# Kernel optimization log

Hardware: AMD Instinct MI355X
Metric: run time of the kernel (lower is better)

Reference implementation:

```python
import jax, jax.numpy as jnp
import numpy as np

N = 100_000
E = 1_600_000
D_IN, D_HID, D_OUT = 512, 256, 256


def setup_inputs() -> dict:
    key = jax.random.key(0)
    ks = jax.random.split(key, 10)
    x = jax.random.normal(ks[0], (N, D_IN), dtype=jnp.float32)
    edge_index = jax.random.randint(ks[1], (2, E), 0, N, dtype=jnp.int64)
    edge_weight = jax.random.uniform(ks[2], (E,), dtype=jnp.float32)
    # Glorot-ish init for the per-layer linear weights (PyG GCNConv: Linear w/o bias, bias added after aggregation)
    W1 = jax.random.normal(ks[3], (D_IN, D_HID), dtype=jnp.float32) * (1.0 / np.sqrt(D_IN))
    b1 = jnp.zeros((D_HID,), dtype=jnp.float32)
    W2 = jax.random.normal(ks[4], (D_HID, D_HID), dtype=jnp.float32) * (1.0 / np.sqrt(D_HID))
    b2 = jnp.zeros((D_HID,), dtype=jnp.float32)
    W3 = jax.random.normal(ks[5], (D_HID, D_OUT), dtype=jnp.float32) * (1.0 / np.sqrt(D_HID))
    b3 = jnp.zeros((D_OUT,), dtype=jnp.float32)
    return {"x": x, "edge_index": edge_index, "edge_weight": edge_weight,
            "W1": W1, "b1": b1, "W2": W2, "b2": b2, "W3": W3, "b3": b3}


def gcn_layer(h_in, W, b, row, col, ew, n):
    # PyG GCNConv with normalize=True, add_self_loops=True (fill value 1.0), aggr='add':
    # h = X W; deg[i] = sum of incoming edge weights (incl. self loop);
    # norm_e = deg^-1/2[row] * w_e * deg^-1/2[col]; out[col] += norm_e * h[row]; out += bias
    h = h_in @ W                                            # [n, d_out]
    deg = jnp.zeros((n,), h.dtype).at[col].add(ew) + 1.0    # +1 from self loop
    dinv = jnp.where(deg > 0, jax.lax.rsqrt(deg), 0.0)      # deg_inv_sqrt, inf -> 0
    norm = dinv[row] * ew * dinv[col]                       # [E]
    out = jnp.zeros_like(h).at[col].add(norm[:, None] * h[row])
    out = out + (dinv * dinv)[:, None] * h                  # self-loop contribution (norm_ii = dinv_i^2)
    return out + b


def reference(x, edge_index, edge_weight, W1, b1, W2, b2, W3, b3):
    row, col = edge_index[0], edge_index[1]
    n = x.shape[0]
    # dropout p=0.0 -> identity
    h = jax.nn.relu(gcn_layer(x, W1, b1, row, col, edge_weight, n))
    h = jax.nn.relu(gcn_layer(h, W2, b2, row, col, edge_weight, n))
    return gcn_layer(h, W3, b3, row, col, edge_weight, n)
```

## Files before the change

### kernel.cpp

```cpp
#include <hip/hip_runtime.h>
#include <hip/hip_bf16.h>


#define D 256
#define ELLW 48
#define BSH 7
#define CAP 2432

typedef unsigned short ushort_t;
typedef unsigned long long u64;
typedef float f32x4 __attribute__((ext_vector_type(4)));
typedef short bf16x8 __attribute__((ext_vector_type(8)));
typedef unsigned int u32x4 __attribute__((ext_vector_type(4)));
typedef int i32x4 __attribute__((ext_vector_type(4)));

__device__ __forceinline__ float blo(unsigned u) { return __uint_as_float(u << 16); }
__device__ __forceinline__ float bhi(unsigned u) { return __uint_as_float(u & 0xFFFF0000u); }
__device__ __forceinline__ ushort_t f2b(float f) {
    unsigned u = __float_as_uint(f);
    return (ushort_t)((u + 0x7FFFu + ((u >> 16) & 1u)) >> 16);
}
__device__ __forceinline__ void gload_lds16(const ushort_t* g, ushort_t* l) {
    __builtin_amdgcn_global_load_lds((const __attribute__((address_space(1))) unsigned int*)g,
                                     (__attribute__((address_space(3))) unsigned int*)l, 16, 0, 0);
}

__global__ __launch_bounds__(256) void bin_p1(const int* __restrict__ row,
                                              const int* __restrict__ col,
                                              const float* __restrict__ ew,
                                              int* __restrict__ bfill,
                                              i32x4* __restrict__ bins, int E) {
    int e = blockIdx.x * 256 + threadIdx.x;
    if (e < E) {
        int c = __builtin_nontemporal_load(&col[e]);
        int r = __builtin_nontemporal_load(&row[e]);
        float w = __builtin_nontemporal_load(&ew[e]);
        int b = c >> BSH;
        int pos = atomicAdd(&bfill[b * 16], 1);
        if (pos < CAP) {
            i32x4 rec = {r, __float_as_int(w), c, 0};
            __builtin_nontemporal_store(rec, &bins[(size_t)b * CAP + pos]);
        }
    }
}

__global__ __launch_bounds__(256) void bin_p2(const i32x4* __restrict__ bins,
                                              const int* __restrict__ bfill,
                                              int* __restrict__ cnt,
                                              float* __restrict__ dinv,
                                              u64* __restrict__ ell, int N) {
    __shared__ int scnt[1 << BSH];
    __shared__ float ssum[1 << BSH];
    const int b = blockIdx.x;
    const int base = b << BSH;
    const int t = threadIdx.x;
    if (t < (1 << BSH)) { scnt[t] = 0; ssum[t] = 0.f; }
    __syncthreads();
    int fill = bfill[b * 16];
    if (fill > CAP) fill = CAP;
    for (int i = t; i < fill; i += 256) {
        i32x4 rec = bins[(size_t)b * CAP + i];
        int li = rec.z - base;
        int pos = atomicAdd(&scnt[li], 1);
        if (pos < ELLW)
            ell[(size_t)rec.z * ELLW + pos] = ((u64)(unsigned)rec.y << 32) | (unsigned)rec.x;
        atomicAdd(&ssum[li], __int_as_float(rec.y));
    }
    __syncthreads();
    if (t < (1 << BSH)) {
        int node = base + t;
        if (node < N) {
            int m = scnt[t];
            cnt[node] = (m > ELLW) ? ELLW : m;
            dinv[node] = rsqrtf(ssum[t] + 1.0f);
        }
    }
}

__global__ __launch_bounds__(256) void cvtT_kernel(const float* __restrict__ W,
                                                   ushort_t* __restrict__ WT, int K, int C) {
    int i = blockIdx.x * 256 + threadIdx.x;
    if (i < K * C) {
        int c = i / K, k = i - c * K;
        WT[i] = f2b(W[(size_t)k * C + c]);
    }
}

template <int K, bool AF32>
__global__ __launch_bounds__(256) void gemm_mfma(const void* __restrict__ Ap,
                                                 const ushort_t* __restrict__ WT,
                                                 ushort_t* __restrict__ C, int nvalid) {
    __shared__ ushort_t As[128 * 64];
    __shared__ ushort_t Bs[256 * 64];
    const int tid = threadIdx.x;
    const int lane = tid & 63, wave = tid >> 6;
    const int wrow = wave >> 1, wcol = wave & 1;
    const int fr = lane & 15, fq = lane >> 4;
    const int r0 = blockIdx.x * 128;

    f32x4 acc[4][8] = {};

    for (int k0 = 0; k0 < K; k0 += 64) {
        if constexpr (AF32) {
            const float* Af = (const float*)Ap;
#pragma unroll
            for (int i = 0; i < 8; ++i) {
                int idx = i * 256 + tid;
                int rowt = idx >> 4;
                int c4 = idx & 15;
                int grow = r0 + rowt;
                if (grow >= nvalid) grow = nvalid - 1;
                f32x4 v = __builtin_nontemporal_load(
                    (const f32x4*)&Af[(size_t)grow * K + k0 + c4 * 4]);
                ushort4 h;
                h.x = f2b(v[0]); h.y = f2b(v[1]); h.z = f2b(v[2]); h.w = f2b(v[3]);
                int slot = c4 >> 1, half = c4 & 1;
                int off = rowt * 64 + ((slot ^ (rowt & 7)) << 3) + (half << 2);
                *(ushort4*)&As[off] = h;
            }
        } else {
            const ushort_t* Ab = (const ushort_t*)Ap;
#pragma unroll
            for (int q = 0; q < 4; ++q) {
                int qa = wave * 4 + q;
                int rowt = qa * 8 + (lane >> 3);
                int g = (lane & 7) ^ (lane >> 3);
                gload_lds16(&Ab[(size_t)(r0 + rowt) * K + k0 + g * 8], &As[qa * 512]);
            }
        }
#pragma unroll
        for (int q = 0; q < 8; ++q) {
            int qb = wave * 8 + q;
            int rowt = qb * 8 + (lane >> 3);
            int g = (lane & 7) ^ (lane >> 3);
            gload_lds16(&WT[(size_t)rowt * K + k0 + g * 8], &Bs[qb * 512]);
        }
        __syncthreads();

#pragma unroll
        for (int kk = 0; kk < 2; ++kk) {
            int g = (kk * 4 + fq) ^ (fr & 7);
            bf16x8 aF[4];
#pragma unroll
            for (int m = 0; m < 4; ++m) {
                int arow = wrow * 64 + m * 16 + fr;
                aF[m] = *(const bf16x8*)&As[arow * 64 + g * 8];
            }
#pragma unroll
            for (int n = 0; n < 8; ++n) {
                int bcol = wcol * 128 + n * 16 + fr;
                bf16x8 bF = *(const bf16x8*)&Bs[bcol * 64 + g * 8];
#pragma unroll
                for (int m = 0; m < 4; ++m)
                    acc[m][n] = __builtin_amdgcn_mfma_f32_16x16x32_bf16(
                        aF[m], bF, acc[m][n], 0, 0, 0);
            }
        }
        __syncthreads();
    }

#pragma unroll
    for (int m = 0; m < 4; ++m) {
        int gr0 = r0 + wrow * 64 + m * 16 + fq * 4;
#pragma unroll
        for (int n = 0; n < 8; ++n) {
            int gc = wcol * 128 + n * 16 + fr;
#pragma unroll
            for (int r = 0; r < 4; ++r) {
                int gr = gr0 + r;
                if (gr < nvalid) C[(size_t)gr * D + gc] = f2b(acc[m][n][r]);
            }
        }
    }
}

template <bool RELU, bool OUTF32>
__global__ __launch_bounds__(256) void agg_kernel(const ushort_t* __restrict__ hb,
                                                  const float* __restrict__ dinv,
                                                  const float* __restrict__ bias,
                                                  const int* __restrict__ cnt,
                                                  const u64* __restrict__ ell,
                                                  void* __restrict__ outp, int N) {
    int node = blockIdx.x * 4 + (threadIdx.x >> 6);
    if (node >= N) return;
    int lane = threadIdx.x & 63;
    int half = lane >> 5;
    int fl = lane & 31;
    float dn = dinv[node], d2 = dn * dn;

    u32x4 sv = *(const u32x4*)&hb[(size_t)node * 256 + fl * 8];
    float sc = half ? 0.f : d2;
    float a0 = sc * blo(sv.x), a1 = sc * bhi(sv.x);
    float a2 = sc * blo(sv.y), a3 = sc * bhi(sv.y);
    float a4 = sc * blo(sv.z), a5 = sc * bhi(sv.z);
    float a6 = sc * blo(sv.w), a7 = sc * bhi(sv.w);

    int m = cnt[node];
    int srcl = 0;
    float wl = 0.f;
    if (lane < m) {
        u64 r = __builtin_nontemporal_load(&ell[(size_t)node * ELLW + lane]);
        srcl = (int)(unsigned)r;
        wl = dinv[srcl] * __uint_as_float((unsigned)(r >> 32)) * dn;
    }
    int steps = (m + 1) >> 1;
#pragma unroll 4
    for (int j = 0; j < steps; ++j) {
        int idx2 = 2 * j + half;
        int src = __shfl(srcl, idx2);
        float w = __shfl(wl, idx2);
        u32x4 v = *(const u32x4*)&hb[(size_t)src * 256 + fl * 8];
        a0 = fmaf(w, blo(v.x), a0); a1 = fmaf(w, bhi(v.x), a1);
        a2 = fmaf(w, blo(v.y), a2); a3 = fmaf(w, bhi(v.y), a3);
        a4 = fmaf(w, blo(v.z), a4); a5 = fmaf(w, bhi(v.z), a5);
        a6 = fmaf(w, blo(v.w), a6); a7 = fmaf(w, bhi(v.w), a7);
    }
    a0 += __shfl_xor(a0, 32); a1 += __shfl_xor(a1, 32);
    a2 += __shfl_xor(a2, 32); a3 += __shfl_xor(a3, 32);
    a4 += __shfl_xor(a4, 32); a5 += __shfl_xor(a5, 32);
    a6 += __shfl_xor(a6, 32); a7 += __shfl_xor(a7, 32);
    float r0 = half ? a4 : a0;
    float r1 = half ? a5 : a1;
    float r2 = half ? a6 : a2;
    float r3 = half ? a7 : a3;
    f32x4 bb = *(const f32x4*)&bias[fl * 8 + half * 4];
    r0 += bb[0]; r1 += bb[1]; r2 += bb[2]; r3 += bb[3];
    if (RELU) {
        r0 = fmaxf(r0, 0.f); r1 = fmaxf(r1, 0.f);
        r2 = fmaxf(r2, 0.f); r3 = fmaxf(r3, 0.f);
    }
    if (OUTF32) {
        f32x4 o = {r0, r1, r2, r3};
        __builtin_nontemporal_store(
            o, (f32x4*)((float*)outp + (size_t)node * 256 + fl * 8 + half * 4));
    } else {
        u64 p = (u64)f2b(r0) | ((u64)f2b(r1) << 16) | ((u64)f2b(r2) << 32) | ((u64)f2b(r3) << 48);
        __builtin_nontemporal_store(
            p, (u64*)((ushort_t*)outp + (size_t)node * 256 + fl * 8 + half * 4));
    }
}

extern "C" void kernel_launch(void* const* d_in, const int* in_sizes, int n_in,
                              void* d_out, int out_size, void* d_ws, size_t ws_size,
                              hipStream_t stream) {
    const float* x  = (const float*)d_in[0];
    const int*   ei = (const int*)d_in[1];
    const float* ew = (const float*)d_in[2];
    const float* W1 = (const float*)d_in[3];
    const float* b1 = (const float*)d_in[4];
    const float* W2 = (const float*)d_in[5];
    const float* b2 = (const float*)d_in[6];
    const float* W3 = (const float*)d_in[7];
    const float* b3 = (const float*)d_in[8];
    const int N = in_sizes[0] / 512;
    const int E = in_sizes[2];
    const int* row = ei;
    const int* col = ei + E;
    float* out = (float*)d_out;

    const int MB = (N + 127) / 128;
    const size_t Npad = (size_t)MB * 128;
    const int NBU = (N + (1 << BSH) - 1) >> BSH;

    char* ws = (char*)d_ws;
    size_t off = 0;
    auto alloc = [&](size_t bytes) -> void* {
        void* p = ws + off;
        off += (bytes + 255) / 256 * 256;
        return p;
    };
    ushort_t* hb  = (ushort_t*)alloc(Npad * D * sizeof(ushort_t));
    u64*      ell = (u64*)alloc((size_t)N * ELLW * sizeof(u64));
    ushort_t* WT1 = (ushort_t*)alloc((size_t)512 * D * sizeof(ushort_t));
    ushort_t* WT2 = (ushort_t*)alloc((size_t)256 * D * sizeof(ushort_t));
    ushort_t* WT3 = (ushort_t*)alloc((size_t)256 * D * sizeof(ushort_t));
    int*   cnt    = (int*)alloc((size_t)N * sizeof(int));
    float* dinv   = (float*)alloc((size_t)N * sizeof(float));
    int*   bfill  = (int*)alloc((size_t)NBU * 16 * sizeof(int));
    i32x4* bins   = (i32x4*)hb;
    ushort_t* ab  = (ushort_t*)d_out;

    (void)hipMemsetAsync(bfill, 0, (size_t)NBU * 16 * sizeof(int), stream);

    int gE = (E + 255) / 256;
    int gA = (N + 3) / 4;
    cvtT_kernel<<<(512 * D + 255) / 256, 256, 0, stream>>>(W1, WT1, 512, D);
    cvtT_kernel<<<(256 * D + 255) / 256, 256, 0, stream>>>(W2, WT2, 256, D);
    cvtT_kernel<<<(256 * D + 255) / 256, 256, 0, stream>>>(W3, WT3, 256, D);
    bin_p1<<<gE, 256, 0, stream>>>(row, col, ew, bfill, bins, E);
    bin_p2<<<NBU, 256, 0, stream>>>(bins, bfill, cnt, dinv, ell, N);

    gemm_mfma<512, true><<<MB, 256, 0, stream>>>(x, WT1, hb, N);
    agg_kernel<true, false><<<gA, 256, 0, stream>>>(hb, dinv, b1, cnt, ell, ab, N);
    gemm_mfma<256, false><<<MB, 256, 0, stream>>>(ab, WT2, hb, N);
    agg_kernel<true, false><<<gA, 256, 0, stream>>>(hb, dinv, b2, cnt, ell, ab, N);
    gemm_mfma<256, false><<<MB, 256, 0, stream>>>(ab, WT3, hb, N);
    agg_kernel<false, true><<<gA, 256, 0, stream>>>(hb, dinv, b3, cnt, ell, out, N);
}
```

Baseline: 727.6 us.

## Shard edge bins, pack LDS atomics, sort ELL rows, widen aggregation gathers

Edge binning now writes to 8 replica sub-bins per bucket, which reduces contention on the global fill-counter atomics. The second pass packs the neighbour count and a fixed-point weight sum into a single 64-bit LDS atomic. A new kernel bitonic-sorts each node's ELL neighbour list by source index, so gathers hit memory in a more local order. The GEMM swaps its MFMA operands so the epilogue can store contiguous ushort4 values, and uses packed bf16 conversion intrinsics. Aggregation moves to 4 edges in flight per wave with 32-byte loads per lane. The tradeoffs are an extra kernel launch and rounding from the fixed-point degree sum.

```diff
diff --git a/kernel.cpp b/kernel.cpp
--- a/kernel.cpp
+++ b/kernel.cpp
@@ -5,13 +5,17 @@
 #define D 256
 #define ELLW 48
 #define BSH 7
-#define CAP 2432
+#define NREP 8
+#define RCAP 352
+#define FIXSCALE 1099511627776.0f
+#define FIXINV   9.094947017729282e-13
 
 typedef unsigned short ushort_t;
 typedef unsigned long long u64;
 typedef float f32x4 __attribute__((ext_vector_type(4)));
 typedef short bf16x8 __attribute__((ext_vector_type(8)));
 typedef unsigned int u32x4 __attribute__((ext_vector_type(4)));
+typedef unsigned int u32x8 __attribute__((ext_vector_type(8)));
 typedef int i32x4 __attribute__((ext_vector_type(4)));
 
 __device__ __forceinline__ float blo(unsigned u) { return __uint_as_float(u << 16); }
@@ -31,15 +35,16 @@
                                               int* __restrict__ bfill,
                                               i32x4* __restrict__ bins, int E) {
     int e = blockIdx.x * 256 + threadIdx.x;
+    int rep = blockIdx.x & (NREP - 1);
     if (e < E) {
         int c = __builtin_nontemporal_load(&col[e]);
         int r = __builtin_nontemporal_load(&row[e]);
         float w = __builtin_nontemporal_load(&ew[e]);
         int b = c >> BSH;
-        int pos = atomicAdd(&bfill[b * 16], 1);
-        if (pos < CAP) {
+        int pos = atomicAdd(&bfill[(b * NREP + rep) * 16], 1);
+        if (pos < RCAP) {
             i32x4 rec = {r, __float_as_int(w), c, 0};
-            __builtin_nontemporal_store(rec, &bins[(size_t)b * CAP + pos]);
+            __builtin_nontemporal_store(rec, &bins[(size_t)b * (NREP * RCAP) + rep * RCAP + pos]);
         }
     }
 }
@@ -49,32 +54,68 @@
                                               int* __restrict__ cnt,
                                               float* __restrict__ dinv,
                                               u64* __restrict__ ell, int N) {
-    __shared__ int scnt[1 << BSH];
-    __shared__ float ssum[1 << BSH];
+    __shared__ u64 sacc[1 << BSH];
     const int b = blockIdx.x;
     const int base = b << BSH;
     const int t = threadIdx.x;
-    if (t < (1 << BSH)) { scnt[t] = 0; ssum[t] = 0.f; }
+    if (t < (1 << BSH)) sacc[t] = 0ull;
     __syncthreads();
-    int fill = bfill[b * 16];
-    if (fill > CAP) fill = CAP;
-    for (int i = t; i < fill; i += 256) {
-        i32x4 rec = bins[(size_t)b * CAP + i];
-        int li = rec.z - base;
-        int pos = atomicAdd(&scnt[li], 1);
-        if (pos < ELLW)
-            ell[(size_t)rec.z * ELLW + pos] = ((u64)(unsigned)rec.y << 32) | (unsigned)rec.x;
-        atomicAdd(&ssum[li], __int_as_float(rec.y));
+#pragma unroll
+    for (int rep = 0; rep < NREP; ++rep) {
+        int fill = bfill[(b * NREP + rep) * 16];
+        if (fill > RCAP) fill = RCAP;
+        for (int i = t; i < fill; i += 256) {
+            i32x4 rec = bins[(size_t)b * (NREP * RCAP) + rep * RCAP + i];
+            int li = rec.z - base;
+            float w = __int_as_float(rec.y);
+            u64 pack = (1ull << 48) | (u64)(w * FIXSCALE);
+            int pos = (int)(atomicAdd(&sacc[li], pack) >> 48);
+            if (pos < ELLW)
+                ell[(size_t)rec.z * ELLW + pos] = ((u64)(unsigned)rec.y << 32) | (unsigned)rec.x;
+        }
     }
     __syncthreads();
     if (t < (1 << BSH)) {
         int node = base + t;
         if (node < N) {
-            int m = scnt[t];
+            u64 p = sacc[t];
+            int m = (int)(p >> 48);
             cnt[node] = (m > ELLW) ? ELLW : m;
-            dinv[node] = rsqrtf(ssum[t] + 1.0f);
-        }
-    }
+            float sum = (float)((double)(p & 0xFFFFFFFFFFFFull) * FIXINV);
+            dinv[node] = rsqrtf(sum + 1.0f);
+        }
+    }
+}
+
+__global__ __launch_bounds__(256) void sort_ell(const int* __restrict__ cnt,
+                                                u64* __restrict__ ell, int N) {
+    int node = blockIdx.x * 4 + (threadIdx.x >> 6);
+    if (node >= N) return;
+    int lane = threadIdx.x & 63;
+    int m = cnt[node];
+    if (m <= 1) return;
+    unsigned key = (0x1FFFFu << 6) | lane;
+    unsigned pw = 0;
+    if (lane < m) {
+        u64 r = ell[(size_t)node * ELLW + lane];
+        key = (((unsigned)r) << 6) | lane;
+        pw = (unsigned)(r >> 32);
+    }
+#pragma unroll
+    for (int k = 2; k <= 64; k <<= 1) {
+#pragma unroll
+        for (int j = k >> 1; j > 0; j >>= 1) {
+            unsigned pkey = __shfl_xor(key, j);
+            unsigned ppw  = __shfl_xor(pw, j);
+            bool dirUp = ((lane & k) == 0);
+            bool lower = ((lane & j) == 0);
+            bool takeOwn = ((key < pkey) == (lower == dirUp));
+            key = takeOwn ? key : pkey;
+            pw  = takeOwn ? pw  : ppw;
+        }
+    }
+    if (lane < m)
+        ell[(size_t)node * ELLW + lane] = (((u64)pw) << 32) | (key >> 6);
 }
 
 __global__ __launch_bounds__(256) void cvtT_kernel(const float* __restrict__ W,
@@ -112,11 +153,12 @@
                 if (grow >= nvalid) grow = nvalid - 1;
                 f32x4 v = __builtin_nontemporal_load(
                     (const f32x4*)&Af[(size_t)grow * K + k0 + c4 * 4]);
-                ushort4 h;
-                h.x = f2b(v[0]); h.y = f2b(v[1]); h.z = f2b(v[2]); h.w = f2b(v[3]);
+                __hip_bfloat162 b01 = __float22bfloat162_rn(make_float2(v[0], v[1]));
+                __hip_bfloat162 b23 = __float22bfloat162_rn(make_float2(v[2], v[3]));
+                uint2 st = make_uint2(*(unsigned*)&b01, *(unsigned*)&b23);
                 int slot = c4 >> 1, half = c4 & 1;
                 int off = rowt * 64 + ((slot ^ (rowt & 7)) << 3) + (half << 2);
-                *(ushort4*)&As[off] = h;
+                *(uint2*)&As[off] = st;
             }
         } else {
             const ushort_t* Ab = (const ushort_t*)Ap;
@@ -153,7 +195,7 @@
 #pragma unroll
                 for (int m = 0; m < 4; ++m)
                     acc[m][n] = __builtin_amdgcn_mfma_f32_16x16x32_bf16(
-                        aF[m], bF, acc[m][n], 0, 0, 0);
+                        bF, aF[m], acc[m][n], 0, 0, 0);
             }
         }
         __syncthreads();
@@ -161,14 +203,14 @@
 
 #pragma unroll
     for (int m = 0; m < 4; ++m) {
-        int gr0 = r0 + wrow * 64 + m * 16 + fq * 4;
-#pragma unroll
-        for (int n = 0; n < 8; ++n) {
-            int gc = wcol * 128 + n * 16 + fr;
-#pragma unroll
-            for (int r = 0; r < 4; ++r) {
-                int gr = gr0 + r;
-                if (gr < nvalid) C[(size_t)gr * D + gc] = f2b(acc[m][n][r]);
+        int gr = r0 + wrow * 64 + m * 16 + fr;
+        if (gr < nvalid) {
+#pragma unroll
+            for (int n = 0; n < 8; ++n) {
+                ushort4 h;
+                h.x = f2b(acc[m][n][0]); h.y = f2b(acc[m][n][1]);
+                h.z = f2b(acc[m][n][2]); h.w = f2b(acc[m][n][3]);
+                *(ushort4*)&C[(size_t)gr * D + wcol * 128 + n * 16 + fq * 4] = h;
             }
         }
     }
@@ -184,46 +226,48 @@
     int node = blockIdx.x * 4 + (threadIdx.x >> 6);
     if (node >= N) return;
     int lane = threadIdx.x & 63;
-    int half = lane >> 5;
-    int fl = lane & 31;
+    int q = lane >> 4;
+    int fl = lane & 15;
     float dn = dinv[node], d2 = dn * dn;
 
-    u32x4 sv = *(const u32x4*)&hb[(size_t)node * 256 + fl * 8];
-    float sc = half ? 0.f : d2;
-    float a0 = sc * blo(sv.x), a1 = sc * bhi(sv.x);
-    float a2 = sc * blo(sv.y), a3 = sc * bhi(sv.y);
-    float a4 = sc * blo(sv.z), a5 = sc * bhi(sv.z);
-    float a6 = sc * blo(sv.w), a7 = sc * bhi(sv.w);
+    u32x8 sv = *(const u32x8*)&hb[(size_t)node * 256 + fl * 16];
+    float sc = (q == 0) ? d2 : 0.f;
+    float a[16];
+#pragma unroll
+    for (int i = 0; i < 8; ++i) { a[2 * i] = sc * blo(sv[i]); a[2 * i + 1] = sc * bhi(sv[i]); }
 
     int m = cnt[node];
     int srcl = 0;
     float wl = 0.f;
     if (lane < m) {
-        u64 r = __builtin_nontemporal_load(&ell[(size_t)node * ELLW + lane]);
+        u64 r = ell[(size_t)node * ELLW + lane];
         srcl = (int)(unsigned)r;
         wl = dinv[srcl] * __uint_as_float((unsigned)(r >> 32)) * dn;
     }
-    int steps = (m + 1) >> 1;
-#pragma unroll 4
+    int steps = (m + 3) >> 2;
+#pragma unroll 2
     for (int j = 0; j < steps; ++j) {
-        int idx2 = 2 * j + half;
-        int src = __shfl(srcl, idx2);
-        float w = __shfl(wl, idx2);
-        u32x4 v = *(const u32x4*)&hb[(size_t)src * 256 + fl * 8];
-        a0 = fmaf(w, blo(v.x), a0); a1 = fmaf(w, bhi(v.x), a1);
-        a2 = fmaf(w, blo(v.y), a2); a3 = fmaf(w, bhi(v.y), a3);
-        a4 = fmaf(w, blo(v.z), a4); a5 = fmaf(w, bhi(v.z), a5);
-        a6 = fmaf(w, blo(v.w), a6); a7 = fmaf(w, bhi(v.w), a7);
-    }
-    a0 += __shfl_xor(a0, 32); a1 += __shfl_xor(a1, 32);
-    a2 += __shfl_xor(a2, 32); a3 += __shfl_xor(a3, 32);
-    a4 += __shfl_xor(a4, 32); a5 += __shfl_xor(a5, 32);
-    a6 += __shfl_xor(a6, 32); a7 += __shfl_xor(a7, 32);
-    float r0 = half ? a4 : a0;
-    float r1 = half ? a5 : a1;
-    float r2 = half ? a6 : a2;
-    float r3 = half ? a7 : a3;
-    f32x4 bb = *(const f32x4*)&bias[fl * 8 + half * 4];
+        int idx = 4 * j + q;
+        int src = __shfl(srcl, idx);
+        float w = __shfl(wl, idx);
+        u32x8 v = *(const u32x8*)&hb[(size_t)src * 256 + fl * 16];
+#pragma unroll
+        for (int i = 0; i < 8; ++i) {
+            a[2 * i]     = fmaf(w, blo(v[i]), a[2 * i]);
+            a[2 * i + 1] = fmaf(w, bhi(v[i]), a[2 * i + 1]);
+        }
+    }
+#pragma unroll
+    for (int i = 0; i < 16; ++i) {
+        a[i] += __shfl_xor(a[i], 16);
+        a[i] += __shfl_xor(a[i], 32);
+    }
+    float r0, r1, r2, r3;
+    if (q == 0)      { r0 = a[0];  r1 = a[1];  r2 = a[2];  r3 = a[3];  }
+    else if (q == 1) { r0 = a[4];  r1 = a[5];  r2 = a[6];  r3 = a[7];  }
+    else if (q == 2) { r0 = a[8];  r1 = a[9];  r2 = a[10]; r3 = a[11]; }
+    else             { r0 = a[12]; r1 = a[13]; r2 = a[14]; r3 = a[15]; }
+    f32x4 bb = *(const f32x4*)&bias[fl * 16 + q * 4];
     r0 += bb[0]; r1 += bb[1]; r2 += bb[2]; r3 += bb[3];
     if (RELU) {
         r0 = fmaxf(r0, 0.f); r1 = fmaxf(r1, 0.f);
@@ -232,11 +276,11 @@
     if (OUTF32) {
         f32x4 o = {r0, r1, r2, r3};
         __builtin_nontemporal_store(
-            o, (f32x4*)((float*)outp + (size_t)node * 256 + fl * 8 + half * 4));
+            o, (f32x4*)((float*)outp + (size_t)node * 256 + fl * 16 + q * 4));
     } else {
         u64 p = (u64)f2b(r0) | ((u64)f2b(r1) << 16) | ((u64)f2b(r2) << 32) | ((u64)f2b(r3) << 48);
         __builtin_nontemporal_store(
-            p, (u64*)((ushort_t*)outp + (size_t)node * 256 + fl * 8 + half * 4));
+            p, (u64*)((ushort_t*)outp + (size_t)node * 256 + fl * 16 + q * 4));
     }
 }
 
@@ -276,11 +320,11 @@
     ushort_t* WT3 = (ushort_t*)alloc((size_t)256 * D * sizeof(ushort_t));
     int*   cnt    = (int*)alloc((size_t)N * sizeof(int));
     float* dinv   = (float*)alloc((size_t)N * sizeof(float));
-    int*   bfill  = (int*)alloc((size_t)NBU * 16 * sizeof(int));
+    int*   bfill  = (int*)alloc((size_t)NBU * NREP * 16 * sizeof(int));
     i32x4* bins   = (i32x4*)hb;
     ushort_t* ab  = (ushort_t*)d_out;
 
-    (void)hipMemsetAsync(bfill, 0, (size_t)NBU * 16 * sizeof(int), stream);
+    (void)hipMemsetAsync(bfill, 0, (size_t)NBU * NREP * 16 * sizeof(int), stream);
 
     int gE = (E + 255) / 256;
     int gA = (N + 3) / 4;
@@ -289,6 +333,7 @@
     cvtT_kernel<<<(256 * D + 255) / 256, 256, 0, stream>>>(W3, WT3, 256, D);
     bin_p1<<<gE, 256, 0, stream>>>(row, col, ew, bfill, bins, E);
     bin_p2<<<NBU, 256, 0, stream>>>(bins, bfill, cnt, dinv, ell, N);
+    sort_ell<<<gA, 256, 0, stream>>>(cnt, ell, N);
 
     gemm_mfma<512, true><<<MB, 256, 0, stream>>>(x, WT1, hb, N);
     agg_kernel<true, false><<<gA, 256, 0, stream>>>(hb, dinv, b1, cnt, ell, ab, N);
```

New measurement: 764.5 us. +5.1%, slower.
